# Kernel tuning notes

Measured on AMD Instinct MI355X. Metric: run time of the kernel, lower is better.

Reference implementation:

```python
import jax, jax.numpy as jnp
import numpy as np

T = 3          # num_node_type
B = 8          # batch
N = 512        # max_doc_len
F_IN = 256     # in_features
F_OUT = 128    # out_features
NE = 10        # num_edge_type (embedding has NE+1 rows, row 0 = padding)
ALPHA = 0.2    # leaky relu slope
NEG = -9e15    # masked-score fill, same constant as torch source


def setup_inputs() -> dict:
    key = jax.random.key(0)
    ks = jax.random.split(key, 7)
    node_rep = jax.random.normal(ks[0], (B, N, F_IN), jnp.float32)
    node_type_mask_rep = jax.random.uniform(ks[1], (T, B, N, 1), jnp.float32)
    adj = jax.random.randint(ks[2], (B, N, N), 0, NE + 1, jnp.int32)
    W = jax.random.normal(ks[3], (T, F_IN, F_OUT), jnp.float32) * 0.05
    b = jnp.zeros((T, F_OUT), jnp.float32)
    # attention vector a in R^{2F} split into halves (GAT trick): a([h_i, x2_ij]) = h_i.a1 + x2_ij.a2 + a_b
    a1 = jax.random.normal(ks[4], (F_OUT,), jnp.float32) * 0.05
    a2 = jax.random.normal(ks[5], (F_OUT,), jnp.float32) * 0.05
    a_b = jnp.zeros((), jnp.float32)
    emb = jax.random.normal(ks[6], (NE + 1, F_OUT), jnp.float32) * 0.05
    emb = emb.at[0].set(0.0)  # padding_idx=0
    return {"node_rep": node_rep, "node_type_mask_rep": node_type_mask_rep,
            "adj": adj, "W": W, "b": b, "a1": a1, "a2": a2, "a_b": a_b, "emb": emb}


def reference(node_rep, node_type_mask_rep, adj, W, b, a1, a2, a_b, emb):
    # typed projection: h = sum_t (node_rep @ W_t + b_t) * mask_t   -> (B, N, F_OUT)
    h = jnp.sum((jnp.einsum('bni,tio->tbno', node_rep, W) + b[:, None, None, :])
                * node_type_mask_rep, axis=0)
    # edge-type embeddings: (B, N, N, F_OUT)
    E = emb[adj]
    # x_2[b,i,j] = h[b,j] + E[b,i,j]
    x2 = h[:, None, :, :] + E
    # score[b,i,j] = leakyrelu(a1.h_i + a2.x2_ij + a_b)  (decomposed concat-linear)
    s = (jnp.einsum('bif,f->bi', h, a1)[:, :, None]
         + jnp.einsum('bijf,f->bij', x2, a2) + a_b)
    s = jnp.where(s > 0, s, ALPHA * s)
    s = jnp.where(adj > 0, s, jnp.float32(NEG))
    attn = jax.nn.softmax(s, axis=2)
    # weighted sum over neighbors of x_2 (NOT h), then ELU
    out = jnp.einsum('bij,bijf->bif', attn, x2)
    return jax.nn.elu(out)
```

## Files before the change

### kernel.cpp

```cpp
#include <hip/hip_runtime.h>

constexpr int kB    = 8;
constexpr int kN    = 512;
constexpr int kFIN  = 256;
constexpr int kFOUT = 128;
constexpr int kNE   = 10;
constexpr int kBN   = kB * kN;
constexpr float kALPHA = 0.2f;
constexpr float kNEG   = -9e15f;

__global__ __launch_bounds__(256) void proj_kernel(
    const float* __restrict__ node_rep,
    const float* __restrict__ mask,
    const float* __restrict__ W,
    const float* __restrict__ bias,
    const float* __restrict__ a1,
    const float* __restrict__ a2,
    const float* __restrict__ a_b,
    const float* __restrict__ emb,
    float* __restrict__ h,
    float* __restrict__ s1,
    float* __restrict__ s2,
    float* __restrict__ emb_a2)
{
    __shared__ float xs[8][kFIN];
    __shared__ float parts[3][3][8][kFOUT];

    const int tid  = threadIdx.x;
    const int row0 = blockIdx.x * 8;
    const int o0   = (tid & 63) * 2;
    const int kq   = tid >> 6;

    #pragma unroll
    for (int it = 0; it < 2; ++it) {
        const int idx = tid + it * 256;
        const int r = idx >> 6, q = idx & 63;
        *(float4*)&xs[r][q * 4] =
            *(const float4*)&node_rep[(size_t)(row0 + r) * kFIN + q * 4];
    }
    __syncthreads();

    float2 acc[3][8];
    #pragma unroll
    for (int t = 0; t < 3; ++t)
        #pragma unroll
        for (int r = 0; r < 8; ++r) acc[t][r] = {0.f, 0.f};

    const float* Wo = W + o0;
    const int k0 = kq * 64;

    #pragma unroll 2
    for (int c = 0; c < 16; ++c) {
        const int kb = k0 + c * 4;
        float2 w[3][4];
        #pragma unroll
        for (int t = 0; t < 3; ++t)
            #pragma unroll
            for (int cc = 0; cc < 4; ++cc)
                w[t][cc] = *(const float2*)&Wo[(size_t)(t * kFIN + kb + cc) * kFOUT];
        float4 xv[8];
        #pragma unroll
        for (int r = 0; r < 8; ++r)
            xv[r] = *(const float4*)&xs[r][kb];
        #pragma unroll
        for (int cc = 0; cc < 4; ++cc)
            #pragma unroll
            for (int r = 0; r < 8; ++r) {
                const float x = ((const float*)&xv[r])[cc];
                acc[0][r].x = fmaf(w[0][cc].x, x, acc[0][r].x);
                acc[0][r].y = fmaf(w[0][cc].y, x, acc[0][r].y);
                acc[1][r].x = fmaf(w[1][cc].x, x, acc[1][r].x);
                acc[1][r].y = fmaf(w[1][cc].y, x, acc[1][r].y);
                acc[2][r].x = fmaf(w[2][cc].x, x, acc[2][r].x);
                acc[2][r].y = fmaf(w[2][cc].y, x, acc[2][r].y);
            }
    }

    if (kq > 0) {
        #pragma unroll
        for (int t = 0; t < 3; ++t)
            #pragma unroll
            for (int r = 0; r < 8; ++r)
                *(float2*)&parts[kq - 1][t][r][o0] = acc[t][r];
    }
    __syncthreads();

    if (kq == 0) {
        #pragma unroll
        for (int r = 0; r < 8; ++r) {
            const int row = row0 + r;
            float2 hv = {0.f, 0.f};
            #pragma unroll
            for (int t = 0; t < 3; ++t) {
                float sx = acc[t][r].x, sy = acc[t][r].y;
                #pragma unroll
                for (int s = 0; s < 3; ++s) {
                    sx += parts[s][t][r][o0];
                    sy += parts[s][t][r][o0 + 1];
                }
                const float2 bt = *(const float2*)&bias[t * kFOUT + o0];
                const float  mt = mask[t * kBN + row];
                hv.x = fmaf(mt, sx + bt.x, hv.x);
                hv.y = fmaf(mt, sy + bt.y, hv.y);
            }
            *(float2*)&h[(size_t)row * kFOUT + o0] = hv;
            *(float2*)&parts[0][0][r][o0] = hv;
        }
    }
    __syncthreads();

    {
        const int wv = tid >> 6, lane = tid & 63;
        #pragma unroll
        for (int rr = 0; rr < 2; ++rr) {
            const int r = wv * 2 + rr;
            const float v0 = parts[0][0][r][lane];
            const float v1 = parts[0][0][r][64 + lane];
            float p1 = v0 * a1[lane] + v1 * a1[64 + lane];
            float p2 = v0 * a2[lane] + v1 * a2[64 + lane];
            #pragma unroll
            for (int off = 32; off; off >>= 1) {
                p1 += __shfl_down(p1, off);
                p2 += __shfl_down(p2, off);
            }
            if (lane == 0) {
                s1[row0 + r] = p1 + a_b[0];
                s2[row0 + r] = p2;
            }
        }
    }

    if (blockIdx.x == 0 && tid < 176) {
        const int e = tid >> 4, l = tid & 15;
        float p = 0.f;
        #pragma unroll
        for (int k8 = 0; k8 < 8; ++k8)
            p += emb[e * kFOUT + l + k8 * 16] * a2[l + k8 * 16];
        #pragma unroll
        for (int off = 8; off; off >>= 1) p += __shfl_xor(p, off);
        if (l == 0) emb_a2[e] = p;
    }
}

__global__ __launch_bounds__(256) void attn_kernel(
    const int*   __restrict__ adj,
    const float* __restrict__ emb,
    const float* __restrict__ h,
    const float* __restrict__ s1,
    const float* __restrict__ s2,
    const float* __restrict__ emb_a2g,
    float* __restrict__ out)
{
    __shared__ float sc[8][kN + 4];
    __shared__ int   adjs[8][kN];
    __shared__ float scT[kN][8];
    __shared__ float wsum[8][16];
    __shared__ float ea2[16];

    const int tid = threadIdx.x;
    const int b   = blockIdx.x >> 6;
    const int i0  = (blockIdx.x & 63) * 8;

    if (tid < 16) ea2[tid] = emb_a2g[tid];
    __syncthreads();

    const int*   adjb = adj + ((size_t)(b * kN + i0)) * kN;
    const float* s2b  = s2 + b * kN;
    #pragma unroll
    for (int it = 0; it < 4; ++it) {
        const int idx = tid + it * 256;
        const int r = idx >> 7, jq = idx & 127;
        const int4   av  = *(const int4*)&adjb[(size_t)r * kN + jq * 4];
        const float4 s2v = *(const float4*)&s2b[jq * 4];
        const float  sr  = s1[b * kN + i0 + r];
        float4 sv; float s;
        s = sr + s2v.x + ea2[av.x]; s = s > 0.f ? s : kALPHA * s; sv.x = av.x > 0 ? s : kNEG;
        s = sr + s2v.y + ea2[av.y]; s = s > 0.f ? s : kALPHA * s; sv.y = av.y > 0 ? s : kNEG;
        s = sr + s2v.z + ea2[av.z]; s = s > 0.f ? s : kALPHA * s; sv.z = av.z > 0 ? s : kNEG;
        s = sr + s2v.w + ea2[av.w]; s = s > 0.f ? s : kALPHA * s; sv.w = av.w > 0 ? s : kNEG;
        *(float4*)&sc[r][jq * 4] = sv;
        *(int4*)&adjs[r][jq * 4] = av;
    }
    __syncthreads();

    {
        const int wv = tid >> 6, lane = tid & 63;
        #pragma unroll
        for (int rr = 0; rr < 2; ++rr) {
            const int r = wv * 2 + rr;
            float v[8]; int av[8];
            #pragma unroll
            for (int k = 0; k < 8; ++k) {
                v[k]  = sc[r][lane + k * 64];
                av[k] = adjs[r][lane + k * 64];
            }
            float m = v[0];
            #pragma unroll
            for (int k = 1; k < 8; ++k) m = fmaxf(m, v[k]);
            #pragma unroll
            for (int off = 32; off; off >>= 1) m = fmaxf(m, __shfl_xor(m, off));
            float sum = 0.f;
            #pragma unroll
            for (int k = 0; k < 8; ++k) { v[k] = __expf(v[k] - m); sum += v[k]; }
            #pragma unroll
            for (int off = 32; off; off >>= 1) sum += __shfl_xor(sum, off);
            const float inv = 1.0f / sum;
            #pragma unroll
            for (int k = 0; k < 8; ++k) {
                v[k] *= inv;
                scT[lane + k * 64][r] = v[k];
            }
            #pragma unroll
            for (int e = 1; e <= kNE; ++e) {
                float p = 0.f;
                #pragma unroll
                for (int k = 0; k < 8; ++k) p += (av[k] == e) ? v[k] : 0.f;
                #pragma unroll
                for (int off = 32; off; off >>= 1) p += __shfl_xor(p, off);
                if (lane == 0) wsum[r][e] = p;
            }
        }
    }
    __syncthreads();

    const int f4l = tid & 31;
    const int rg  = (tid >> 5) & 1;
    const int js  = tid >> 6;
    const float* hb  = h + ((size_t)(b * kN + js * 128)) * kFOUT + f4l * 4;
    const float* sct = &scT[js * 128][rg * 4];

    float4 acc0 = {0,0,0,0}, acc1 = {0,0,0,0}, acc2 = {0,0,0,0}, acc3 = {0,0,0,0};
    #pragma unroll 4
    for (int jj = 0; jj < 128; ++jj) {
        const float4 w4 = *(const float4*)&sct[jj * 8];
        const float4 hv = *(const float4*)&hb[(size_t)jj * kFOUT];
        acc0.x = fmaf(w4.x, hv.x, acc0.x); acc0.y = fmaf(w4.x, hv.y, acc0.y);
        acc0.z = fmaf(w4.x, hv.z, acc0.z); acc0.w = fmaf(w4.x, hv.w, acc0.w);
        acc1.x = fmaf(w4.y, hv.x, acc1.x); acc1.y = fmaf(w4.y, hv.y, acc1.y);
        acc1.z = fmaf(w4.y, hv.z, acc1.z); acc1.w = fmaf(w4.y, hv.w, acc1.w);
        acc2.x = fmaf(w4.z, hv.x, acc2.x); acc2.y = fmaf(w4.z, hv.y, acc2.y);
        acc2.z = fmaf(w4.z, hv.z, acc2.z); acc2.w = fmaf(w4.z, hv.w, acc2.w);
        acc3.x = fmaf(w4.w, hv.x, acc3.x); acc3.y = fmaf(w4.w, hv.y, acc3.y);
        acc3.z = fmaf(w4.w, hv.z, acc3.z); acc3.w = fmaf(w4.w, hv.w, acc3.w);
    }
    __syncthreads();

    float* parts = (float*)adjs;
    {
        const int rbase = rg * 4;
        *(float4*)&parts[((js * 8) + rbase + 0) * kFOUT + f4l * 4] = acc0;
        *(float4*)&parts[((js * 8) + rbase + 1) * kFOUT + f4l * 4] = acc1;
        *(float4*)&parts[((js * 8) + rbase + 2) * kFOUT + f4l * 4] = acc2;
        *(float4*)&parts[((js * 8) + rbase + 3) * kFOUT + f4l * 4] = acc3;
    }
    __syncthreads();

    {
        const int r  = tid >> 5;
        const int fl = (tid & 31) * 4;
        float4 a = {0,0,0,0};
        #pragma unroll
        for (int p = 0; p < 4; ++p) {
            const float4 pv = *(const float4*)&parts[((p * 8) + r) * kFOUT + fl];
            a.x += pv.x; a.y += pv.y; a.z += pv.z; a.w += pv.w;
        }
        #pragma unroll
        for (int e = 1; e <= kNE; ++e) {
            const float  wv = wsum[r][e];
            const float4 ev = *(const float4*)&emb[e * kFOUT + fl];
            a.x = fmaf(wv, ev.x, a.x); a.y = fmaf(wv, ev.y, a.y);
            a.z = fmaf(wv, ev.z, a.z); a.w = fmaf(wv, ev.w, a.w);
        }
        a.x = a.x > 0.f ? a.x : expm1f(a.x);
        a.y = a.y > 0.f ? a.y : expm1f(a.y);
        a.z = a.z > 0.f ? a.z : expm1f(a.z);
        a.w = a.w > 0.f ? a.w : expm1f(a.w);
        *(float4*)&out[((size_t)(b * kN + i0 + r)) * kFOUT + fl] = a;
    }
}

extern "C" void kernel_launch(void* const* d_in, const int* in_sizes, int n_in,
                              void* d_out, int out_size, void* d_ws, size_t ws_size,
                              hipStream_t stream) {
    const float* node_rep = (const float*)d_in[0];
    const float* mask     = (const float*)d_in[1];
    const int*   adj      = (const int*)  d_in[2];
    const float* W        = (const float*)d_in[3];
    const float* bias     = (const float*)d_in[4];
    const float* a1       = (const float*)d_in[5];
    const float* a2       = (const float*)d_in[6];
    const float* a_b      = (const float*)d_in[7];
    const float* emb      = (const float*)d_in[8];
    float* out = (float*)d_out;

    float* ws     = (float*)d_ws;
    float* h      = ws;
    float* s1     = h + (size_t)kBN * kFOUT;
    float* s2     = s1 + kBN;
    float* emb_a2 = s2 + kBN;

    proj_kernel<<<kBN / 8, 256, 0, stream>>>(
        node_rep, mask, W, bias, a1, a2, a_b, emb, h, s1, s2, emb_a2);
    attn_kernel<<<kBN / 8, 256, 0, stream>>>(
        adj, emb, h, s1, s2, emb_a2, out);
}
```

Baseline: 114.3 us.

## Split projection K across blocks with reduce kernel; widen attention blocks to 512 threads

```diff
diff --git a/kernel.cpp b/kernel.cpp
--- a/kernel.cpp
+++ b/kernel.cpp
@@ -9,10 +9,97 @@
 constexpr float kALPHA = 0.2f;
 constexpr float kNEG   = -9e15f;
 
-__global__ __launch_bounds__(256) void proj_kernel(
+__global__ __launch_bounds__(128) void proj_kernel(
     const float* __restrict__ node_rep,
     const float* __restrict__ mask,
     const float* __restrict__ W,
+    float* __restrict__ part)
+{
+    __shared__ float xs[8][64];
+    __shared__ float pcomb[3][8][kFOUT];
+
+    const int tid  = threadIdx.x;
+    const int rb   = blockIdx.x >> 2;
+    const int sl   = blockIdx.x & 3;
+    const int row0 = rb * 8;
+    const int k0   = sl * 64;
+
+    {
+        const int r = tid >> 4, q = tid & 15;
+        *(float4*)&xs[r][q * 4] =
+            *(const float4*)&node_rep[(size_t)(row0 + r) * kFIN + k0 + q * 4];
+    }
+    __syncthreads();
+
+    const int o0 = (tid & 63) * 2;
+    const int kh = tid >> 6;
+
+    float2 acc[3][8];
+    #pragma unroll
+    for (int t = 0; t < 3; ++t)
+        #pragma unroll
+        for (int r = 0; r < 8; ++r) acc[t][r] = {0.f, 0.f};
+
+    const float* Wo = W + o0;
+
+    #pragma unroll
+    for (int c = 0; c < 8; ++c) {
+        const int kb = kh * 32 + c * 4;
+        float2 w[3][4];
+        #pragma unroll
+        for (int t = 0; t < 3; ++t)
+            #pragma unroll
+            for (int cc = 0; cc < 4; ++cc)
+                w[t][cc] = *(const float2*)&Wo[(size_t)(t * kFIN + k0 + kb + cc) * kFOUT];
+        float4 xv[8];
+        #pragma unroll
+        for (int r = 0; r < 8; ++r)
+            xv[r] = *(const float4*)&xs[r][kb];
+        #pragma unroll
+        for (int cc = 0; cc < 4; ++cc)
+            #pragma unroll
+            for (int r = 0; r < 8; ++r) {
+                const float x = ((const float*)&xv[r])[cc];
+                acc[0][r].x = fmaf(w[0][cc].x, x, acc[0][r].x);
+                acc[0][r].y = fmaf(w[0][cc].y, x, acc[0][r].y);
+                acc[1][r].x = fmaf(w[1][cc].x, x, acc[1][r].x);
+                acc[1][r].y = fmaf(w[1][cc].y, x, acc[1][r].y);
+                acc[2][r].x = fmaf(w[2][cc].x, x, acc[2][r].x);
+                acc[2][r].y = fmaf(w[2][cc].y, x, acc[2][r].y);
+            }
+    }
+
+    if (kh == 1) {
+        #pragma unroll
+        for (int t = 0; t < 3; ++t)
+            #pragma unroll
+            for (int r = 0; r < 8; ++r)
+                *(float2*)&pcomb[t][r][o0] = acc[t][r];
+    }
+    __syncthreads();
+
+    if (kh == 0) {
+        #pragma unroll
+        for (int r = 0; r < 8; ++r) {
+            const int row = row0 + r;
+            const float m0 = mask[0 * kBN + row];
+            const float m1 = mask[1 * kBN + row];
+            const float m2 = mask[2 * kBN + row];
+            float2 pv;
+            pv.x = m0 * (acc[0][r].x + pcomb[0][r][o0])
+                 + m1 * (acc[1][r].x + pcomb[1][r][o0])
+                 + m2 * (acc[2][r].x + pcomb[2][r][o0]);
+            pv.y = m0 * (acc[0][r].y + pcomb[0][r][o0 + 1])
+                 + m1 * (acc[1][r].y + pcomb[1][r][o0 + 1])
+                 + m2 * (acc[2][r].y + pcomb[2][r][o0 + 1]);
+            *(float2*)&part[((size_t)sl * kBN + row) * kFOUT + o0] = pv;
+        }
+    }
+}
+
+__global__ __launch_bounds__(256) void reduce_kernel(
+    const float* __restrict__ part,
+    const float* __restrict__ mask,
     const float* __restrict__ bias,
     const float* __restrict__ a1,
     const float* __restrict__ a2,
@@ -23,89 +110,26 @@
     float* __restrict__ s2,
     float* __restrict__ emb_a2)
 {
-    __shared__ float xs[8][kFIN];
-    __shared__ float parts[3][3][8][kFOUT];
+    __shared__ float hls[8][kFOUT];
 
     const int tid  = threadIdx.x;
     const int row0 = blockIdx.x * 8;
-    const int o0   = (tid & 63) * 2;
-    const int kq   = tid >> 6;
+    const int o    = tid & 127;
+    const int rh   = tid >> 7;
 
     #pragma unroll
-    for (int it = 0; it < 2; ++it) {
-        const int idx = tid + it * 256;
-        const int r = idx >> 6, q = idx & 63;
-        *(float4*)&xs[r][q * 4] =
-            *(const float4*)&node_rep[(size_t)(row0 + r) * kFIN + q * 4];
-    }
-    __syncthreads();
-
-    float2 acc[3][8];
-    #pragma unroll
-    for (int t = 0; t < 3; ++t)
-        #pragma unroll
-        for (int r = 0; r < 8; ++r) acc[t][r] = {0.f, 0.f};
-
-    const float* Wo = W + o0;
-    const int k0 = kq * 64;
-
-    #pragma unroll 2
-    for (int c = 0; c < 16; ++c) {
-        const int kb = k0 + c * 4;
-        float2 w[3][4];
-        #pragma unroll
-        for (int t = 0; t < 3; ++t)
-            #pragma unroll
-            for (int cc = 0; cc < 4; ++cc)
-                w[t][cc] = *(const float2*)&Wo[(size_t)(t * kFIN + kb + cc) * kFOUT];
-        float4 xv[8];
-        #pragma unroll
-        for (int r = 0; r < 8; ++r)
-            xv[r] = *(const float4*)&xs[r][kb];
-        #pragma unroll
-        for (int cc = 0; cc < 4; ++cc)
-            #pragma unroll
-            for (int r = 0; r < 8; ++r) {
-                const float x = ((const float*)&xv[r])[cc];
-                acc[0][r].x = fmaf(w[0][cc].x, x, acc[0][r].x);
-                acc[0][r].y = fmaf(w[0][cc].y, x, acc[0][r].y);
-                acc[1][r].x = fmaf(w[1][cc].x, x, acc[1][r].x);
-                acc[1][r].y = fmaf(w[1][cc].y, x, acc[1][r].y);
-                acc[2][r].x = fmaf(w[2][cc].x, x, acc[2][r].x);
-                acc[2][r].y = fmaf(w[2][cc].y, x, acc[2][r].y);
-            }
-    }
-
-    if (kq > 0) {
-        #pragma unroll
-        for (int t = 0; t < 3; ++t)
-            #pragma unroll
-            for (int r = 0; r < 8; ++r)
-                *(float2*)&parts[kq - 1][t][r][o0] = acc[t][r];
-    }
-    __syncthreads();
-
-    if (kq == 0) {
-        #pragma unroll
-        for (int r = 0; r < 8; ++r) {
-            const int row = row0 + r;
-            float2 hv = {0.f, 0.f};
-            #pragma unroll
-            for (int t = 0; t < 3; ++t) {
-                float sx = acc[t][r].x, sy = acc[t][r].y;
-                #pragma unroll
-                for (int s = 0; s < 3; ++s) {
-                    sx += parts[s][t][r][o0];
-                    sy += parts[s][t][r][o0 + 1];
-                }
-                const float2 bt = *(const float2*)&bias[t * kFOUT + o0];
-                const float  mt = mask[t * kBN + row];
-                hv.x = fmaf(mt, sx + bt.x, hv.x);
-                hv.y = fmaf(mt, sy + bt.y, hv.y);
-            }
-            *(float2*)&h[(size_t)row * kFOUT + o0] = hv;
-            *(float2*)&parts[0][0][r][o0] = hv;
-        }
+    for (int rr = 0; rr < 4; ++rr) {
+        const int r   = rh * 4 + rr;
+        const int row = row0 + r;
+        float hv = part[((size_t)0 * kBN + row) * kFOUT + o]
+                 + part[((size_t)1 * kBN + row) * kFOUT + o]
+                 + part[((size_t)2 * kBN + row) * kFOUT + o]
+                 + part[((size_t)3 * kBN + row) * kFOUT + o];
+        hv += mask[0 * kBN + row] * bias[0 * kFOUT + o]
+            + mask[1 * kBN + row] * bias[1 * kFOUT + o]
+            + mask[2 * kBN + row] * bias[2 * kFOUT + o];
+        h[(size_t)row * kFOUT + o] = hv;
+        hls[r][o] = hv;
     }
     __syncthreads();
 
@@ -114,8 +138,8 @@
         #pragma unroll
         for (int rr = 0; rr < 2; ++rr) {
             const int r = wv * 2 + rr;
-            const float v0 = parts[0][0][r][lane];
-            const float v1 = parts[0][0][r][64 + lane];
+            const float v0 = hls[r][lane];
+            const float v1 = hls[r][64 + lane];
             float p1 = v0 * a1[lane] + v1 * a1[64 + lane];
             float p2 = v0 * a2[lane] + v1 * a2[64 + lane];
             #pragma unroll
@@ -142,7 +166,7 @@
     }
 }
 
-__global__ __launch_bounds__(256) void attn_kernel(
+__global__ __launch_bounds__(512) void attn_kernel(
     const int*   __restrict__ adj,
     const float* __restrict__ emb,
     const float* __restrict__ h,
@@ -167,8 +191,8 @@
     const int*   adjb = adj + ((size_t)(b * kN + i0)) * kN;
     const float* s2b  = s2 + b * kN;
     #pragma unroll
-    for (int it = 0; it < 4; ++it) {
-        const int idx = tid + it * 256;
+    for (int it = 0; it < 2; ++it) {
+        const int idx = tid + it * 512;
         const int r = idx >> 7, jq = idx & 127;
         const int4   av  = *(const int4*)&adjb[(size_t)r * kN + jq * 4];
         const float4 s2v = *(const float4*)&s2b[jq * 4];
@@ -184,41 +208,37 @@
     __syncthreads();
 
     {
-        const int wv = tid >> 6, lane = tid & 63;
-        #pragma unroll
-        for (int rr = 0; rr < 2; ++rr) {
-            const int r = wv * 2 + rr;
-            float v[8]; int av[8];
-            #pragma unroll
-            for (int k = 0; k < 8; ++k) {
-                v[k]  = sc[r][lane + k * 64];
-                av[k] = adjs[r][lane + k * 64];
-            }
-            float m = v[0];
-            #pragma unroll
-            for (int k = 1; k < 8; ++k) m = fmaxf(m, v[k]);
-            #pragma unroll
-            for (int off = 32; off; off >>= 1) m = fmaxf(m, __shfl_xor(m, off));
-            float sum = 0.f;
-            #pragma unroll
-            for (int k = 0; k < 8; ++k) { v[k] = __expf(v[k] - m); sum += v[k]; }
-            #pragma unroll
-            for (int off = 32; off; off >>= 1) sum += __shfl_xor(sum, off);
-            const float inv = 1.0f / sum;
-            #pragma unroll
-            for (int k = 0; k < 8; ++k) {
-                v[k] *= inv;
-                scT[lane + k * 64][r] = v[k];
-            }
-            #pragma unroll
-            for (int e = 1; e <= kNE; ++e) {
-                float p = 0.f;
-                #pragma unroll
-                for (int k = 0; k < 8; ++k) p += (av[k] == e) ? v[k] : 0.f;
-                #pragma unroll
-                for (int off = 32; off; off >>= 1) p += __shfl_xor(p, off);
-                if (lane == 0) wsum[r][e] = p;
-            }
+        const int r = tid >> 6, lane = tid & 63;
+        float v[8]; int av[8];
+        #pragma unroll
+        for (int k = 0; k < 8; ++k) {
+            v[k]  = sc[r][lane + k * 64];
+            av[k] = adjs[r][lane + k * 64];
+        }
+        float m = v[0];
+        #pragma unroll
+        for (int k = 1; k < 8; ++k) m = fmaxf(m, v[k]);
+        #pragma unroll
+        for (int off = 32; off; off >>= 1) m = fmaxf(m, __shfl_xor(m, off));
+        float sum = 0.f;
+        #pragma unroll
+        for (int k = 0; k < 8; ++k) { v[k] = __expf(v[k] - m); sum += v[k]; }
+        #pragma unroll
+        for (int off = 32; off; off >>= 1) sum += __shfl_xor(sum, off);
+        const float inv = 1.0f / sum;
+        #pragma unroll
+        for (int k = 0; k < 8; ++k) {
+            v[k] *= inv;
+            scT[lane + k * 64][r] = v[k];
+        }
+        #pragma unroll
+        for (int e = 1; e <= kNE; ++e) {
+            float p = 0.f;
+            #pragma unroll
+            for (int k = 0; k < 8; ++k) p += (av[k] == e) ? v[k] : 0.f;
+            #pragma unroll
+            for (int off = 32; off; off >>= 1) p += __shfl_xor(p, off);
+            if (lane == 0) wsum[r][e] = p;
         }
     }
     __syncthreads();
@@ -226,12 +246,12 @@
     const int f4l = tid & 31;
     const int rg  = (tid >> 5) & 1;
     const int js  = tid >> 6;
-    const float* hb  = h + ((size_t)(b * kN + js * 128)) * kFOUT + f4l * 4;
-    const float* sct = &scT[js * 128][rg * 4];
+    const float* hb  = h + ((size_t)(b * kN + js * 64)) * kFOUT + f4l * 4;
+    const float* sct = &scT[js * 64][rg * 4];
 
     float4 acc0 = {0,0,0,0}, acc1 = {0,0,0,0}, acc2 = {0,0,0,0}, acc3 = {0,0,0,0};
     #pragma unroll 4
-    for (int jj = 0; jj < 128; ++jj) {
+    for (int jj = 0; jj < 64; ++jj) {
         const float4 w4 = *(const float4*)&sct[jj * 8];
         const float4 hv = *(const float4*)&hb[(size_t)jj * kFOUT];
         acc0.x = fmaf(w4.x, hv.x, acc0.x); acc0.y = fmaf(w4.x, hv.y, acc0.y);
@@ -245,24 +265,29 @@
     }
     __syncthreads();
 
-    float* parts = (float*)adjs;
+    float* parts_lo = (float*)adjs;
+    float* parts_hi = (float*)sc;
     {
+        float* pbase = (js < 4) ? parts_lo + js * 1024
+                                : parts_hi + (js - 4) * 1024;
         const int rbase = rg * 4;
-        *(float4*)&parts[((js * 8) + rbase + 0) * kFOUT + f4l * 4] = acc0;
-        *(float4*)&parts[((js * 8) + rbase + 1) * kFOUT + f4l * 4] = acc1;
-        *(float4*)&parts[((js * 8) + rbase + 2) * kFOUT + f4l * 4] = acc2;
-        *(float4*)&parts[((js * 8) + rbase + 3) * kFOUT + f4l * 4] = acc3;
-    }
-    __syncthreads();
-
-    {
+        *(float4*)&pbase[(rbase + 0) * kFOUT + f4l * 4] = acc0;
+        *(float4*)&pbase[(rbase + 1) * kFOUT + f4l * 4] = acc1;
+        *(float4*)&pbase[(rbase + 2) * kFOUT + f4l * 4] = acc2;
+        *(float4*)&pbase[(rbase + 3) * kFOUT + f4l * 4] = acc3;
+    }
+    __syncthreads();
+
+    if (tid < 256) {
         const int r  = tid >> 5;
         const int fl = (tid & 31) * 4;
         float4 a = {0,0,0,0};
         #pragma unroll
         for (int p = 0; p < 4; ++p) {
-            const float4 pv = *(const float4*)&parts[((p * 8) + r) * kFOUT + fl];
-            a.x += pv.x; a.y += pv.y; a.z += pv.z; a.w += pv.w;
+            const float4 v0 = *(const float4*)&parts_lo[p * 1024 + r * kFOUT + fl];
+            const float4 v1 = *(const float4*)&parts_hi[p * 1024 + r * kFOUT + fl];
+            a.x += v0.x + v1.x; a.y += v0.y + v1.y;
+            a.z += v0.z + v1.z; a.w += v0.w + v1.w;
         }
         #pragma unroll
         for (int e = 1; e <= kNE; ++e) {
@@ -298,9 +323,11 @@
     float* s1     = h + (size_t)kBN * kFOUT;
     float* s2     = s1 + kBN;
     float* emb_a2 = s2 + kBN;
-
-    proj_kernel<<<kBN / 8, 256, 0, stream>>>(
-        node_rep, mask, W, bias, a1, a2, a_b, emb, h, s1, s2, emb_a2);
-    attn_kernel<<<kBN / 8, 256, 0, stream>>>(
+    float* part   = emb_a2 + 16;
+
+    proj_kernel<<<2048, 128, 0, stream>>>(node_rep, mask, W, part);
+    reduce_kernel<<<kBN / 8, 256, 0, stream>>>(
+        part, mask, bias, a1, a2, a_b, emb, h, s1, s2, emb_a2);
+    attn_kernel<<<kBN / 8, 512, 0, stream>>>(
         adj, emb, h, s1, s2, emb_a2, out);
 }
```

After: 111.6 us. -2.4%, faster.
